# Kernel tuning notes

Hardware: AMD Instinct MI355X
Metric: run time of the kernel (lower is better)

Reference implementation:

```python
import jax, jax.numpy as jnp
import numpy as np

# EKV transistor-model constants (from the torch module)
EKV_ALPHA = 0.0005625
EKV_N = 1.5
EKV_VD = 0.1
EKV_VT = 0.025
K = 3       # kernel_size
STRIDE = 1
PAD = 1
INIT_THETA_MEAN = 4.5
INIT_THETA_STD = 0.5


def setup_inputs() -> dict:
    key = jax.random.key(0)
    k1, k2 = jax.random.split(key)
    V_in = jax.random.normal(k1, (4, 64, 32, 32), dtype=jnp.float32)
    theta = INIT_THETA_MEAN + INIT_THETA_STD * jax.random.normal(
        k2, (128, 64, K, K), dtype=jnp.float32)
    return {"V_in": V_in, "theta": theta}


def _ekv_conv(V_in, theta):
    # V_in: [B, Cin, H, W]; theta: [Cout, Cin, K, K]
    B, Cin, H, W = V_in.shape
    Cout = theta.shape[0]
    Ho = (H + 2 * PAD - K) // STRIDE + 1
    Wo = (W + 2 * PAD - K) // STRIDE + 1
    Vp = jnp.pad(V_in, ((0, 0), (0, 0), (PAD, PAD), (PAD, PAD)))
    inv = 1.0 / (2.0 * EKV_N * EKV_VT)
    out = jnp.zeros((B, Cout, Ho, Wo), dtype=V_in.dtype)
    # Loop over the K*K kernel taps (fixed, small) instead of materializing
    # the full [B, Cout, L, Cin*K*K] unfold intermediate.
    for i in range(K):
        for j in range(K):
            # shifted input window: [B, Cin, Ho, Wo]
            patch = Vp[:, :, i:i + STRIDE * Ho:STRIDE, j:j + STRIDE * Wo:STRIDE]
            th = theta[:, :, i, j]                     # [Cout, Cin]
            # V_diff: [B, Cout, Cin, Ho, Wo]
            Vd = patch[:, None, :, :, :] - th[None, :, :, None, None]
            t1 = jax.nn.softplus(Vd * inv) ** 2
            t2 = jax.nn.softplus((Vd - EKV_VD) * inv) ** 2
            out = out + EKV_ALPHA * jnp.sum(t1 - t2, axis=2)
    return out


def reference(V_in, theta):
    return _ekv_conv(V_in, theta)
```

## Files before the change

### kernel.cpp

```cpp
#include <hip/hip_runtime.h>


constexpr int CIN  = 64;
constexpr int COUT = 128;
constexpr int HW   = 32;
constexpr int PIX  = HW * HW;

constexpr float S     = 19.235933878519512f;
constexpr float KF    = 0.26359713811572677f;
constexpr float OSC   = 2.7025482032899376e-4f;
constexpr float DELTA = 0.4158883f;

__global__ __launch_bounds__(256)
void ekv_rowmax(const float* __restrict__ V, float* __restrict__ wg)
{
    const int t = threadIdx.x;
    const int plane = blockIdx.x;
    __shared__ float rmax[32];
    const float4 v4 = reinterpret_cast<const float4*>(V + (size_t)plane * PIX)[t];
    float m = fmaxf(fmaxf(v4.x, v4.y), fmaxf(v4.z, v4.w));
    m = fmaxf(m, __shfl_xor(m, 1));
    m = fmaxf(m, __shfl_xor(m, 2));
    m = fmaxf(m, __shfl_xor(m, 4));
    if ((t & 7) == 0) rmax[t >> 3] = m;
    __syncthreads();
    if (t < 4) {
        float wm = 0.0f;
        #pragma unroll
        for (int rr = 0; rr < 10; ++rr) {
            const int r = 8 * t - 1 + rr;
            if (r >= 0 && r < 32) wm = fmaxf(wm, rmax[r]);
        }
        wg[plane * 4 + t] = wm;
    }
}

__global__ __launch_bounds__(256, 4)
void ekv_main(const float* __restrict__ V, const float* __restrict__ Th,
              const float* __restrict__ wg, float* __restrict__ Out)
{
    const int t = threadIdx.x;
    const int task  = ((blockIdx.x & 7) << 8) | (blockIdx.x >> 3);
    const int win   = task & 3;
    const int co    = (task >> 2) & (COUT - 1);
    const int b     = task >> 9;
    const int phase = t >> 6;
    const int lane  = t & 63;

    __shared__ float  Qs[CIN * 9];
    __shared__ float  Ts[CIN];
    __shared__ float4 Cb[256];

    const float* vbase = V  + (size_t)b  * CIN * PIX;
    const float* thp   = Th + (size_t)co * (CIN * 9);

    for (int i = t; i < CIN * 9; i += 256)
        Qs[i] = __builtin_amdgcn_exp2f(-thp[i] * S);

    float thmin = 1e30f;
    #pragma unroll
    for (int k = 0; k < 9; ++k) thmin = fminf(thmin, thp[lane * 9 + k]);
    const float wgv = wg[(size_t)(b * CIN + lane) * 4 + win];
    const unsigned long long full = __ballot(wgv >= thmin - DELTA);

    if (t < CIN) Ts[t] = __builtin_amdgcn_exp2f(-8.0f - wgv * S);

    const bool actv = (full >> lane) & 1ull;
    const int  rank = (int)__popcll(full & ((1ull << lane) - 1ull));
    unsigned long long mask = __ballot(actv && ((rank & 3) == phase));

    __syncthreads();

    const int lr = lane >> 3;
    const int lc = (lane & 7) * 4;
    const int r   = 8 * win + lr;
    const int rm1 = (r - 1 < 0)  ? 0  : r - 1;
    const int rp1 = (r + 1 > 31) ? 31 : r + 1;
    const bool okA = (r - 1) >= 0;
    const bool okC = (r + 1) <= 31;
    const bool isL = (lane & 7) == 0;
    const bool isR = (lane & 7) == 7;
    const int  lcl = isL ? 0 : lc - 1;
    const int  lcr = isR ? 31 : lc + 4;

    float acc0 = 0.f, acc1 = 0.f, acc2 = 0.f, acc3 = 0.f;

    auto pop = [&]() -> int {
        if (!mask) return -1;
        const int c = (int)__builtin_ctzll(mask); mask &= mask - 1; return c;
    };
    auto issue = [&](int cin, float4& A, float4& B, float4& C,
                     float2& eA, float2& eB, float2& eC) {
        const float* src = vbase + cin * PIX;
        const float* ra = src + rm1 * HW;
        const float* rb = src + r   * HW;
        const float* rc = src + rp1 * HW;
        A = *reinterpret_cast<const float4*>(ra + lc);
        B = *reinterpret_cast<const float4*>(rb + lc);
        C = *reinterpret_cast<const float4*>(rc + lc);
        eA.x = ra[lcl]; eA.y = ra[lcr];
        eB.x = rb[lcl]; eB.y = rb[lcr];
        eC.x = rc[lcl]; eC.y = rc[lcr];
    };
    auto rowv = [&](const float4& x, const float2& e, bool ok, float* vals) {
        vals[0] = __builtin_amdgcn_exp2f(((ok && !isL) ? e.x : 0.f) * S);
        vals[1] = __builtin_amdgcn_exp2f((ok ? x.x : 0.f) * S);
        vals[2] = __builtin_amdgcn_exp2f((ok ? x.y : 0.f) * S);
        vals[3] = __builtin_amdgcn_exp2f((ok ? x.z : 0.f) * S);
        vals[4] = __builtin_amdgcn_exp2f((ok ? x.w : 0.f) * S);
        vals[5] = __builtin_amdgcn_exp2f(((ok && !isR) ? e.y : 0.f) * S);
    };
    auto compute = [&](int cin, const float4& A, const float4& B, const float4& C,
                       const float2& eA, const float2& eB, const float2& eC) {
        const float  T  = Ts[cin];
        const float* qp = &Qs[cin * 9];
        #pragma unroll
        for (int i = 0; i < 3; ++i) {
            const float q0 = qp[i * 3 + 0];
            const float q1 = qp[i * 3 + 1];
            const float q2 = qp[i * 3 + 2];
            if (fmaxf(fmaxf(q0, q1), q2) < T) continue;
            float vals[6];
            if      (i == 0) rowv(A, eA, okA, vals);
            else if (i == 1) rowv(B, eB, true, vals);
            else             rowv(C, eC, okC, vals);
            #pragma unroll
            for (int j = 0; j < 3; ++j) {
                const float qa = (j == 0) ? q0 : (j == 1) ? q1 : q2;
                if (qa < T) continue;
                const float qb = qa * KF;
                #pragma unroll
                for (int k = 0; k < 4; ++k) {
                    const float x1 = __builtin_fmaf(vals[k + j], qa, 1.0f);
                    const float x2 = __builtin_fmaf(vals[k + j], qb, 1.0f);
                    const float l1 = __builtin_amdgcn_logf(x1);
                    const float l2 = __builtin_amdgcn_logf(x2);
                    const float su = l1 + l2, di = l1 - l2;
                    if      (k == 0) acc0 = __builtin_fmaf(su, di, acc0);
                    else if (k == 1) acc1 = __builtin_fmaf(su, di, acc1);
                    else if (k == 2) acc2 = __builtin_fmaf(su, di, acc2);
                    else             acc3 = __builtin_fmaf(su, di, acc3);
                }
            }
        }
    };

    {
        float4 aA = make_float4(0.f,0.f,0.f,0.f), bA = aA, cA = aA;
        float4 aB = aA, bB = aA, cB = aA;
        float2 eaA = make_float2(0.f,0.f), ebA = eaA, ecA = eaA;
        float2 eaB = eaA, ebB = eaA, ecB = eaA;
        int q0 = pop();
        if (q0 >= 0) {
            issue(q0, aA, bA, cA, eaA, ebA, ecA);
            int q1 = pop();
            if (q1 >= 0) issue(q1, aB, bB, cB, eaB, ebB, ecB);
            for (;;) {
                {
                    const float4 xa = aA, xb = bA, xc = cA;
                    const float2 ya = eaA, yb = ebA, yc = ecA;
                    int q2 = pop();
                    if (q2 >= 0) issue(q2, aA, bA, cA, eaA, ebA, ecA);
                    compute(q0, xa, xb, xc, ya, yb, yc);
                    if (q1 < 0) break;
                    q0 = q2;
                }
                {
                    const float4 xa = aB, xb = bB, xc = cB;
                    const float2 ya = eaB, yb = ebB, yc = ecB;
                    int q3 = pop();
                    if (q3 >= 0) issue(q3, aB, bB, cB, eaB, ebB, ecB);
                    compute(q1, xa, xb, xc, ya, yb, yc);
                    if (q0 < 0) break;
                    q1 = q3;
                }
            }
        }
    }

    Cb[t] = make_float4(acc0, acc1, acc2, acc3);
    __syncthreads();
    if (t < 64) {
        const float4 p0 = Cb[t];
        const float4 p1 = Cb[t + 64];
        const float4 p2 = Cb[t + 128];
        const float4 p3 = Cb[t + 192];
        float4 o;
        o.x = (p0.x + p1.x + p2.x + p3.x) * OSC;
        o.y = (p0.y + p1.y + p2.y + p3.y) * OSC;
        o.z = (p0.z + p1.z + p2.z + p3.z) * OSC;
        o.w = (p0.w + p1.w + p2.w + p3.w) * OSC;
        float* obase = Out + (size_t)(b * COUT + co) * PIX + win * 256;
        reinterpret_cast<float4*>(obase)[t] = o;
    }
}

extern "C" void kernel_launch(void* const* d_in, const int* in_sizes, int n_in,
                              void* d_out, int out_size, void* d_ws, size_t ws_size,
                              hipStream_t stream) {
    (void)in_sizes; (void)n_in; (void)ws_size; (void)out_size;
    const float* V  = (const float*)d_in[0];
    const float* Th = (const float*)d_in[1];
    float* Out = (float*)d_out;
    float* wg  = (float*)d_ws;
    ekv_rowmax<<<dim3(4 * CIN), dim3(256), 0, stream>>>(V, wg);
    ekv_main<<<dim3(4 * COUT * 4), dim3(256), 0, stream>>>(V, Th, wg, Out);
}
```

Before: 29.25 us.

## Use dynamic LDS work queue and per-row activity masks for channel pruning

```diff
diff --git a/kernel.cpp b/kernel.cpp
--- a/kernel.cpp
+++ b/kernel.cpp
@@ -44,12 +44,14 @@
     const int win   = task & 3;
     const int co    = (task >> 2) & (COUT - 1);
     const int b     = task >> 9;
-    const int phase = t >> 6;
     const int lane  = t & 63;
 
-    __shared__ float  Qs[CIN * 9];
-    __shared__ float  Ts[CIN];
-    __shared__ float4 Cb[256];
+    __shared__ float    Qs[CIN * 9];
+    __shared__ float    Ts[CIN];
+    __shared__ unsigned rlm[CIN];
+    __shared__ int      listS[80];
+    __shared__ int      nactS, headS;
+    __shared__ float4   Cb[256];
 
     const float* vbase = V  + (size_t)b  * CIN * PIX;
     const float* thp   = Th + (size_t)co * (CIN * 9);
@@ -57,19 +59,29 @@
     for (int i = t; i < CIN * 9; i += 256)
         Qs[i] = __builtin_amdgcn_exp2f(-thp[i] * S);
 
-    float thmin = 1e30f;
-    #pragma unroll
-    for (int k = 0; k < 9; ++k) thmin = fminf(thmin, thp[lane * 9 + k]);
-    const float wgv = wg[(size_t)(b * CIN + lane) * 4 + win];
-    const unsigned long long full = __ballot(wgv >= thmin - DELTA);
-
-    if (t < CIN) Ts[t] = __builtin_amdgcn_exp2f(-8.0f - wgv * S);
-
-    const bool actv = (full >> lane) & 1ull;
-    const int  rank = (int)__popcll(full & ((1ull << lane) - 1ull));
-    unsigned long long mask = __ballot(actv && ((rank & 3) == phase));
+    if (t < CIN) {
+        const float wgv = wg[(size_t)(b * CIN + t) * 4 + win];
+        const float lim = wgv + DELTA;
+        float m0 = 1e30f, m1 = 1e30f, m2 = 1e30f;
+        #pragma unroll
+        for (int k = 0; k < 3; ++k) m0 = fminf(m0, thp[t * 9 + k]);
+        #pragma unroll
+        for (int k = 3; k < 6; ++k) m1 = fminf(m1, thp[t * 9 + k]);
+        #pragma unroll
+        for (int k = 6; k < 9; ++k) m2 = fminf(m2, thp[t * 9 + k]);
+        const unsigned rm = (m0 <= lim ? 1u : 0u) | (m1 <= lim ? 2u : 0u)
+                          | (m2 <= lim ? 4u : 0u);
+        rlm[t] = rm;
+        Ts[t]  = __builtin_amdgcn_exp2f(-8.0f - wgv * S);
+        const bool act = rm != 0u;
+        const unsigned long long bal = __ballot(act);
+        const int rank = (int)__popcll(bal & ((1ull << t) - 1ull));
+        if (act) listS[rank] = t;
+        if (t == 0) { nactS = (int)__popcll(bal); headS = 0; }
+    }
 
     __syncthreads();
+    const int nact = nactS;
 
     const int lr = lane >> 3;
     const int lc = (lane & 7) * 4;
@@ -86,21 +98,30 @@
     float acc0 = 0.f, acc1 = 0.f, acc2 = 0.f, acc3 = 0.f;
 
     auto pop = [&]() -> int {
-        if (!mask) return -1;
-        const int c = (int)__builtin_ctzll(mask); mask &= mask - 1; return c;
+        int idx = 0;
+        if (lane == 0) idx = atomicAdd(&headS, 1);
+        idx = __shfl(idx, 0);
+        return (idx < nact) ? listS[idx] : -1;
     };
     auto issue = [&](int cin, float4& A, float4& B, float4& C,
                      float2& eA, float2& eB, float2& eC) {
+        const unsigned m = rlm[cin];
         const float* src = vbase + cin * PIX;
-        const float* ra = src + rm1 * HW;
-        const float* rb = src + r   * HW;
-        const float* rc = src + rp1 * HW;
-        A = *reinterpret_cast<const float4*>(ra + lc);
-        B = *reinterpret_cast<const float4*>(rb + lc);
-        C = *reinterpret_cast<const float4*>(rc + lc);
-        eA.x = ra[lcl]; eA.y = ra[lcr];
-        eB.x = rb[lcl]; eB.y = rb[lcr];
-        eC.x = rc[lcl]; eC.y = rc[lcr];
+        if (m & 1u) {
+            const float* ra = src + rm1 * HW;
+            A = *reinterpret_cast<const float4*>(ra + lc);
+            eA.x = ra[lcl]; eA.y = ra[lcr];
+        }
+        if (m & 2u) {
+            const float* rb = src + r * HW;
+            B = *reinterpret_cast<const float4*>(rb + lc);
+            eB.x = rb[lcl]; eB.y = rb[lcr];
+        }
+        if (m & 4u) {
+            const float* rc = src + rp1 * HW;
+            C = *reinterpret_cast<const float4*>(rc + lc);
+            eC.x = rc[lcl]; eC.y = rc[lcr];
+        }
     };
     auto rowv = [&](const float4& x, const float2& e, bool ok, float* vals) {
         vals[0] = __builtin_amdgcn_exp2f(((ok && !isL) ? e.x : 0.f) * S);
@@ -112,14 +133,15 @@
     };
     auto compute = [&](int cin, const float4& A, const float4& B, const float4& C,
                        const float2& eA, const float2& eB, const float2& eC) {
-        const float  T  = Ts[cin];
-        const float* qp = &Qs[cin * 9];
+        const float    T  = Ts[cin];
+        const unsigned m  = rlm[cin];
+        const float*   qp = &Qs[cin * 9];
         #pragma unroll
         for (int i = 0; i < 3; ++i) {
+            if (!((m >> i) & 1u)) continue;
             const float q0 = qp[i * 3 + 0];
             const float q1 = qp[i * 3 + 1];
             const float q2 = qp[i * 3 + 2];
-            if (fmaxf(fmaxf(q0, q1), q2) < T) continue;
             float vals[6];
             if      (i == 0) rowv(A, eA, okA, vals);
             else if (i == 1) rowv(B, eB, true, vals);
@@ -159,7 +181,7 @@
                 {
                     const float4 xa = aA, xb = bA, xc = cA;
                     const float2 ya = eaA, yb = ebA, yc = ecA;
-                    int q2 = pop();
+                    int q2 = (q1 >= 0) ? pop() : -1;
                     if (q2 >= 0) issue(q2, aA, bA, cA, eaA, ebA, ecA);
                     compute(q0, xa, xb, xc, ya, yb, yc);
                     if (q1 < 0) break;
@@ -168,7 +190,7 @@
                 {
                     const float4 xa = aB, xb = bB, xc = cB;
                     const float2 ya = eaB, yb = ebB, yc = ecB;
-                    int q3 = pop();
+                    int q3 = (q0 >= 0) ? pop() : -1;
                     if (q3 >= 0) issue(q3, aB, bB, cB, eaB, ebB, ecB);
                     compute(q1, xa, xb, xc, ya, yb, yc);
                     if (q0 < 0) break;
```

New measurement: 25.72 us. 12.1% less time.
